# Performance work log

Hardware: AMD Instinct MI355X
Metric: run time of the kernel (lower is better)

## Reference

```python
import jax, jax.numpy as jnp
import numpy as np

NUM_RELS = 19


def rgcn_layer(h, W, b, src, dst, etype, n_nodes):
    """DGL RelGraphConv (basis regularizer, num_bases=num_rels, sum aggregation, bias, no self-loop).

    out[v] = sum_{e: dst(e)=v} W[etype(e)] @ h[src(e)] + b
    Computed as: aggregate h[src] per (relation, dst) pair, then one GEMM per relation.
    """
    # segment id combines relation and destination node -> [R*N] segments
    seg = etype * n_nodes + dst
    agg = jax.ops.segment_sum(h[src], seg, num_segments=NUM_RELS * n_nodes)
    agg = agg.reshape(NUM_RELS, n_nodes, h.shape[1])  # [R, N, in]
    return jnp.einsum('rni,rio->no', agg, W) + b       # [N, out]


def setup_inputs() -> dict:
    key = jax.random.key(0)
    ks = jax.random.split(key, 8)
    N, E, R, D = 100000, 1600000, NUM_RELS, 32
    s = 0.1  # keep activations well-scaled across layers
    return {
        'src': jax.random.randint(ks[0], (E,), 0, N, dtype=jnp.int32),
        'dst': jax.random.randint(ks[1], (E,), 0, N, dtype=jnp.int32),
        'etype': jax.random.randint(ks[2], (E,), 0, R, dtype=jnp.int32),
        'n_nodes': N,
        'W1': jax.random.normal(ks[3], (R, 1, D), jnp.float32) * s,
        'b1': jnp.zeros((D,), jnp.float32),
        'W2': jax.random.normal(ks[4], (R, D, D), jnp.float32) * s,
        'b2': jnp.zeros((D,), jnp.float32),
        'W3': jax.random.normal(ks[5], (D, D), jnp.float32) * s,
        'b3': jnp.zeros((D,), jnp.float32),
    }


def reference(src, dst, etype, n_nodes, W1, b1, W2, b2, W3, b3):
    # h = ones(N, 1), as in Embedder.forward
    h = jnp.ones((n_nodes, 1), jnp.float32)
    h = jax.nn.relu(rgcn_layer(h, W1, b1, src, dst, etype, n_nodes))
    h = jax.nn.relu(rgcn_layer(h, W2, b2, src, dst, etype, n_nodes))
    # conv_output=False -> final layer is a plain Linear
    return h @ W3 + b3
```

## Files before the change

kernel.cpp:

```cpp
#include <hip/hip_runtime.h>

#define NUM_RELS 19
#define NPB 256
#define NPB_SHIFT 8
#define MAXB 400
#define NBLK 512

typedef _Float16 half8 __attribute__((ext_vector_type(8)));
typedef float floatx4 __attribute__((ext_vector_type(4)));



__global__ void w2swz_kernel(const float* __restrict__ W2, _Float16* __restrict__ W2F,
                             int* __restrict__ bcnt, int B) {
    int idx = blockIdx.x * blockDim.x + threadIdx.x;
    if (idx < B) bcnt[idx] = 0;
    if (idx >= NUM_RELS * 2 * 64 * 8) return;
    int j = idx & 7, lane = (idx >> 3) & 63, nt = (idx >> 9) & 1, r = idx >> 10;
    int k = (lane >> 4) * 8 + j, n = nt * 16 + (lane & 15);
    W2F[idx] = (_Float16)W2[r * 1024 + k * 32 + n];
}


__global__ __launch_bounds__(512) void count_kernel(const int* __restrict__ dst,
                                                    int* __restrict__ blkhist,
                                                    int* __restrict__ bcnt,
                                                    int E, int B, int chunk) {
    __shared__ int h[MAXB];
    for (int i = threadIdx.x; i < B; i += 512) h[i] = 0;
    __syncthreads();
    int e0 = blockIdx.x * chunk, e1 = min(E, e0 + chunk);
    for (int e = e0 + (int)threadIdx.x; e < e1; e += 512)
        atomicAdd(&h[dst[e] >> NPB_SHIFT], 1);
    __syncthreads();
    for (int i = threadIdx.x; i < B; i += 512) {
        blkhist[blockIdx.x * B + i] = h[i];
        if (h[i]) atomicAdd(&bcnt[i], h[i]);
    }
}


__global__ __launch_bounds__(NBLK) void offscan_kernel(const int* __restrict__ blkhist,
                                                       const int* __restrict__ bcnt,
                                                       int* __restrict__ pbase,
                                                       int* __restrict__ offs, int B) {
    __shared__ int lds[NBLK];
    __shared__ int pbs;
    int bucket = blockIdx.x;
    int t = threadIdx.x;

    int c = (t < B) ? ((bcnt[t] + 7) & ~7) : 0;
    lds[t] = c;
    __syncthreads();
    for (int off = 1; off < NBLK; off <<= 1) {
        int x = (t >= off) ? lds[t - off] : 0;
        __syncthreads();
        lds[t] += x;
        __syncthreads();
    }
    if (t == bucket) {
        pbs = lds[t] - c;
        pbase[bucket] = pbs;
    }
    __syncthreads();
    int myp = pbs;

    int v = blkhist[t * B + bucket];
    lds[t] = v;
    __syncthreads();
    for (int off = 1; off < NBLK; off <<= 1) {
        int x = (t >= off) ? lds[t - off] : 0;
        __syncthreads();
        lds[t] += x;
        __syncthreads();
    }
    offs[t * B + bucket] = myp + lds[t] - v;
}


__global__ __launch_bounds__(512) void scatter2_kernel(
    const int* __restrict__ src, const int* __restrict__ dst, const int* __restrict__ etype,
    const int* __restrict__ offs, unsigned* __restrict__ recs4, int E, int B, int chunk) {
    __shared__ int cur[MAXB];
    for (int i = threadIdx.x; i < B; i += 512) cur[i] = offs[blockIdx.x * B + i];
    __syncthreads();
    int e0 = blockIdx.x * chunk, e1 = min(E, e0 + chunk);
    for (int e = e0 + (int)threadIdx.x; e < e1; e += 512) {
        int d = dst[e];
        int b = d >> NPB_SHIFT;
        int pos = atomicAdd(&cur[b], 1);
        recs4[pos] = ((unsigned)(d & (NPB - 1)) << 22) | ((unsigned)src[e] << 5) | (unsigned)etype[e];
    }
}


__global__ __launch_bounds__(256) void bsort_l1_kernel(
    const unsigned* __restrict__ recs4, const int* __restrict__ pbase, const int* __restrict__ bcnt,
    int* __restrict__ recs2, int* __restrict__ row_start, int* __restrict__ rend,
    const float* __restrict__ W1, const float* __restrict__ b1, _Float16* __restrict__ h1, int N) {
    __shared__ int hist[NPB];
    __shared__ int offsl[NPB];
    __shared__ int cur[NPB];
    __shared__ int cnt2[NPB * NUM_RELS];
    __shared__ float W1s[NUM_RELS * 32];
    __shared__ float b1s[32];
    int b = blockIdx.x;
    int p0 = pbase[b], n = bcnt[b];
    int t = threadIdx.x;

    hist[t] = 0;
    for (int i = t; i < NPB * NUM_RELS; i += 256) cnt2[i] = 0;
    for (int i = t; i < NUM_RELS * 32; i += 256) W1s[i] = W1[i];
    if (t < 32) b1s[t] = b1[t];
    __syncthreads();

    for (int i = t; i < n; i += 256) {
        unsigned rec = recs4[p0 + i];
        int ln = rec >> 22;
        atomicAdd(&hist[ln], 1);
        atomicAdd(&cnt2[ln * NUM_RELS + (rec & 31)], 1);
    }
    __syncthreads();
    int c = hist[t];
    offsl[t] = c;
    __syncthreads();
    for (int off = 1; off < 256; off <<= 1) {
        int x = (t >= off) ? offsl[t - off] : 0;
        __syncthreads();
        offsl[t] += x;
        __syncthreads();
    }
    int start = p0 + offsl[t] - c;
    cur[t] = start;
    int v = (b << NPB_SHIFT) + t;
    if (v < N) {
        row_start[v] = start;
        rend[v] = start + c;
    }
    __syncthreads();
    for (int i = t; i < n; i += 256) {
        unsigned rec = recs4[p0 + i];
        int p = atomicAdd(&cur[rec >> 22], 1);
        recs2[p] = (int)(rec & 0x3FFFFFu);
    }

    int o = t & 31, hw = t >> 5;
    int v0 = b << NPB_SHIFT;
    for (int k = hw; k < NPB; k += 8) {
        int vv = v0 + k;
        if (vv >= N) break;
        float acc = b1s[o];
        const int* cp = &cnt2[k * NUM_RELS];
#pragma unroll
        for (int r = 0; r < NUM_RELS; ++r) acc += (float)cp[r] * W1s[r * 32 + o];
        h1[(size_t)vv * 32 + o] = (_Float16)fmaxf(acc, 0.f);
    }
}


__global__ __launch_bounds__(256) void transform_kernel(
    const _Float16* __restrict__ h1, const _Float16* __restrict__ W2F,
    _Float16* __restrict__ g, int N) {
    int lane = threadIdx.x & 63;
    int tile = blockIdx.x * 4 + (threadIdx.x >> 6);
    int v0 = tile * 16;
    if (v0 >= N) return;

    half8 a = *(const half8*)(h1 + (size_t)(v0 + (lane & 15)) * 32 + (lane >> 4) * 8);

    floatx4 zero = {0.f, 0.f, 0.f, 0.f};
    int row = (lane >> 4) * 4;
    int col = lane & 15;
    for (int r = 0; r < NUM_RELS; ++r) {
        _Float16* gbase = g + ((size_t)r * N + v0) * 32;
#pragma unroll
        for (int nt = 0; nt < 2; ++nt) {
            half8 bfrag = *(const half8*)(W2F + ((r * 2 + nt) * 64 + lane) * 8);
            floatx4 d = __builtin_amdgcn_mfma_f32_16x16x32_f16(a, bfrag, zero, 0, 0, 0);
#pragma unroll
            for (int reg = 0; reg < 4; ++reg) {
                gbase[(row + reg) * 32 + nt * 16 + col] = (_Float16)d[reg];
            }
        }
    }
}


__global__ __launch_bounds__(512) void edge23_kernel(
    const _Float16* __restrict__ g, const int* __restrict__ row_start,
    const int* __restrict__ rend, const int* __restrict__ recs2,
    const float* __restrict__ b2, const float* __restrict__ W3, const float* __restrict__ b3,
    float* __restrict__ out, int N) {
    __shared__ float W3s[1024];
    __shared__ float b2s[32], b3s[32];
    for (int i = threadIdx.x; i < 1024; i += 512) W3s[i] = W3[i];
    if (threadIdx.x < 32) {
        b2s[threadIdx.x] = b2[threadIdx.x];
        b3s[threadIdx.x] = b3[threadIdx.x];
    }
    __syncthreads();

    int o = threadIdx.x & 31;
    int hw = blockIdx.x * 16 + (threadIdx.x >> 5);
    if (hw >= N) return;
    int start = row_start[hw], end = rend[hw];
    const int sN32 = N * 32;

    float acc = b2s[o];
    for (int base = start; base < end; base += 32) {
        int idx = base + o;
        int m_l = (idx < end) ? recs2[idx] : 0;
        int cnt = min(32, end - base);
        int j = 0;
        for (; j + 4 <= cnt; j += 4) {
            float x[4];
#pragma unroll
            for (int k = 0; k < 4; ++k) {
                int m = __shfl(m_l, j + k, 32);
                x[k] = (float)g[(m & 31) * sN32 + (m >> 5) * 32 + o];
            }
            acc += ((x[0] + x[1]) + (x[2] + x[3]));
        }
        for (; j < cnt; ++j) {
            int m = __shfl(m_l, j, 32);
            acc += (float)g[(m & 31) * sN32 + (m >> 5) * 32 + o];
        }
    }
    float h2v = fmaxf(acc, 0.f);

    float acc3 = b3s[o];
#pragma unroll
    for (int i = 0; i < 32; ++i) {
        float hi = __shfl(h2v, i, 32);
        acc3 = fmaf(hi, W3s[i * 32 + o], acc3);
    }
    out[(size_t)hw * 32 + o] = acc3;
}


extern "C" void kernel_launch(void* const* d_in, const int* in_sizes, int n_in,
                              void* d_out, int out_size, void* d_ws, size_t ws_size,
                              hipStream_t stream) {
    const int* src   = (const int*)d_in[0];
    const int* dst   = (const int*)d_in[1];
    const int* etype = (const int*)d_in[2];
    const float* W1  = (const float*)d_in[4];
    const float* b1  = (const float*)d_in[5];
    const float* W2  = (const float*)d_in[6];
    const float* b2  = (const float*)d_in[7];
    const float* W3  = (const float*)d_in[8];
    const float* b3  = (const float*)d_in[9];
    float* out = (float*)d_out;

    int E = in_sizes[0];
    int N = out_size / 32;
    int B = (N + NPB - 1) >> NPB_SHIFT;

    char* ws = (char*)d_ws;
    size_t off = 0;
    auto alloc = [&](size_t bytes) {
        void* p = ws + off;
        off = (off + bytes + 255) & ~(size_t)255;
        return p;
    };
    _Float16* h1    = (_Float16*)alloc((size_t)N * 32 * 2);
    int* bcnt       = (int*)alloc((size_t)MAXB * 4);
    int* pbase      = (int*)alloc((size_t)MAXB * 4);
    int* blkhist    = (int*)alloc((size_t)NBLK * MAXB * 4);
    int* offs       = (int*)alloc((size_t)NBLK * MAXB * 4);
    int* row_start  = (int*)alloc((size_t)N * 4);
    int* rend       = (int*)alloc((size_t)N * 4);
    unsigned* recs4 = (unsigned*)alloc(((size_t)E + 8 * MAXB + 64) * 4);
    int* recs2      = (int*)alloc(((size_t)E + 8 * MAXB + 64) * 4);
    _Float16* g     = (_Float16*)alloc((size_t)NUM_RELS * N * 32 * 2);
    _Float16* W2F   = (_Float16*)alloc((size_t)NUM_RELS * 2 * 64 * 8 * 2);

    w2swz_kernel<<<(NUM_RELS * 2 * 64 * 8 + 255) / 256, 256, 0, stream>>>(W2, W2F, bcnt, B);

    int chunk = (E + NBLK - 1) / NBLK;
    count_kernel<<<NBLK, 512, 0, stream>>>(dst, blkhist, bcnt, E, B, chunk);
    offscan_kernel<<<B, NBLK, 0, stream>>>(blkhist, bcnt, pbase, offs, B);
    scatter2_kernel<<<NBLK, 512, 0, stream>>>(src, dst, etype, offs, recs4, E, B, chunk);

    bsort_l1_kernel<<<B, 256, 0, stream>>>(recs4, pbase, bcnt, recs2, row_start, rend,
                                           W1, b1, h1, N);

    int ntiles = (N + 15) / 16;
    transform_kernel<<<(ntiles + 3) / 4, 256, 0, stream>>>(h1, W2F, g, N);

    edge23_kernel<<<(N + 15) / 16, 512, 0, stream>>>(g, row_start, rend, recs2, b2, W3, b3, out, N);
}
```

Measured before the change: 230.8 us.

## Fuse layer-1 bucket sort and per-relation transform into one kernel

Merges the bucket-sort/layer-1 kernel with the MFMA transform kernel, so the h1 tile stays in shared memory instead of making a round trip through global memory. This also removes one launch. The fused kernel grows to 512 threads per block. Only B≈391 blocks now do the g-write work that was previously spread over many more blocks, which lowers parallelism for the store-heavy transform stage.

```diff
diff --git a/kernel.cpp b/kernel.cpp
--- a/kernel.cpp
+++ b/kernel.cpp
@@ -94,92 +94,95 @@
 }
 
 
-__global__ __launch_bounds__(256) void bsort_l1_kernel(
+__global__ __launch_bounds__(512) void bsort_l1t_kernel(
     const unsigned* __restrict__ recs4, const int* __restrict__ pbase, const int* __restrict__ bcnt,
     int* __restrict__ recs2, int* __restrict__ row_start, int* __restrict__ rend,
-    const float* __restrict__ W1, const float* __restrict__ b1, _Float16* __restrict__ h1, int N) {
+    const float* __restrict__ W1, const float* __restrict__ b1,
+    const _Float16* __restrict__ W2F, _Float16* __restrict__ g, int N) {
     __shared__ int hist[NPB];
     __shared__ int offsl[NPB];
     __shared__ int cur[NPB];
     __shared__ int cnt2[NPB * NUM_RELS];
     __shared__ float W1s[NUM_RELS * 32];
     __shared__ float b1s[32];
+    __shared__ _Float16 h1t[NPB * 32];
     int b = blockIdx.x;
     int p0 = pbase[b], n = bcnt[b];
     int t = threadIdx.x;
 
-    hist[t] = 0;
-    for (int i = t; i < NPB * NUM_RELS; i += 256) cnt2[i] = 0;
-    for (int i = t; i < NUM_RELS * 32; i += 256) W1s[i] = W1[i];
+    if (t < NPB) hist[t] = 0;
+    for (int i = t; i < NPB * NUM_RELS; i += 512) cnt2[i] = 0;
+    for (int i = t; i < NUM_RELS * 32; i += 512) W1s[i] = W1[i];
     if (t < 32) b1s[t] = b1[t];
     __syncthreads();
 
-    for (int i = t; i < n; i += 256) {
+    for (int i = t; i < n; i += 512) {
         unsigned rec = recs4[p0 + i];
         int ln = rec >> 22;
         atomicAdd(&hist[ln], 1);
         atomicAdd(&cnt2[ln * NUM_RELS + (rec & 31)], 1);
     }
     __syncthreads();
-    int c = hist[t];
-    offsl[t] = c;
-    __syncthreads();
-    for (int off = 1; off < 256; off <<= 1) {
-        int x = (t >= off) ? offsl[t - off] : 0;
-        __syncthreads();
-        offsl[t] += x;
-        __syncthreads();
-    }
-    int start = p0 + offsl[t] - c;
-    cur[t] = start;
-    int v = (b << NPB_SHIFT) + t;
-    if (v < N) {
-        row_start[v] = start;
-        rend[v] = start + c;
-    }
-    __syncthreads();
-    for (int i = t; i < n; i += 256) {
+    int c = 0;
+    if (t < NPB) {
+        c = hist[t];
+        offsl[t] = c;
+    }
+    __syncthreads();
+    for (int off = 1; off < NPB; off <<= 1) {
+        int x = 0;
+        if (t < NPB && t >= off) x = offsl[t - off];
+        __syncthreads();
+        if (t < NPB) offsl[t] += x;
+        __syncthreads();
+    }
+    if (t < NPB) {
+        int start = p0 + offsl[t] - c;
+        cur[t] = start;
+        int v = (b << NPB_SHIFT) + t;
+        if (v < N) {
+            row_start[v] = start;
+            rend[v] = start + c;
+        }
+    }
+    __syncthreads();
+    for (int i = t; i < n; i += 512) {
         unsigned rec = recs4[p0 + i];
         int p = atomicAdd(&cur[rec >> 22], 1);
         recs2[p] = (int)(rec & 0x3FFFFFu);
     }
 
     int o = t & 31, hw = t >> 5;
-    int v0 = b << NPB_SHIFT;
-    for (int k = hw; k < NPB; k += 8) {
-        int vv = v0 + k;
-        if (vv >= N) break;
+    int v0n = b << NPB_SHIFT;
+    for (int k = hw; k < NPB; k += 16) {
+        int vv = v0n + k;
         float acc = b1s[o];
         const int* cp = &cnt2[k * NUM_RELS];
 #pragma unroll
         for (int r = 0; r < NUM_RELS; ++r) acc += (float)cp[r] * W1s[r * 32 + o];
-        h1[(size_t)vv * 32 + o] = (_Float16)fmaxf(acc, 0.f);
-    }
-}
-
-
-__global__ __launch_bounds__(256) void transform_kernel(
-    const _Float16* __restrict__ h1, const _Float16* __restrict__ W2F,
-    _Float16* __restrict__ g, int N) {
-    int lane = threadIdx.x & 63;
-    int tile = blockIdx.x * 4 + (threadIdx.x >> 6);
-    int v0 = tile * 16;
-    if (v0 >= N) return;
-
-    half8 a = *(const half8*)(h1 + (size_t)(v0 + (lane & 15)) * 32 + (lane >> 4) * 8);
-
+        h1t[k * 32 + o] = (vv < N) ? (_Float16)fmaxf(acc, 0.f) : (_Float16)0.f;
+    }
+    __syncthreads();
+
+    int lane = t & 63;
+    int wv = t >> 6;
     floatx4 zero = {0.f, 0.f, 0.f, 0.f};
     int row = (lane >> 4) * 4;
     int col = lane & 15;
-    for (int r = 0; r < NUM_RELS; ++r) {
-        _Float16* gbase = g + ((size_t)r * N + v0) * 32;
-#pragma unroll
-        for (int nt = 0; nt < 2; ++nt) {
-            half8 bfrag = *(const half8*)(W2F + ((r * 2 + nt) * 64 + lane) * 8);
-            floatx4 d = __builtin_amdgcn_mfma_f32_16x16x32_f16(a, bfrag, zero, 0, 0, 0);
-#pragma unroll
-            for (int reg = 0; reg < 4; ++reg) {
-                gbase[(row + reg) * 32 + nt * 16 + col] = (_Float16)d[reg];
+    for (int tile = wv; tile < NPB / 16; tile += 8) {
+        int v0g = v0n + tile * 16;
+        if (v0g >= N) continue;
+        half8 a = *(const half8*)(h1t + (tile * 16 + (lane & 15)) * 32 + (lane >> 4) * 8);
+        for (int r = 0; r < NUM_RELS; ++r) {
+            _Float16* gbase = g + ((size_t)r * N + v0g) * 32;
+#pragma unroll
+            for (int nt = 0; nt < 2; ++nt) {
+                half8 bfrag = *(const half8*)(W2F + ((r * 2 + nt) * 64 + lane) * 8);
+                floatx4 d = __builtin_amdgcn_mfma_f32_16x16x32_f16(a, bfrag, zero, 0, 0, 0);
+#pragma unroll
+                for (int reg = 0; reg < 4; ++reg) {
+                    gbase[(row + reg) * 32 + nt * 16 + col] = (_Float16)d[reg];
+                }
             }
         }
     }
@@ -263,7 +266,6 @@
         off = (off + bytes + 255) & ~(size_t)255;
         return p;
     };
-    _Float16* h1    = (_Float16*)alloc((size_t)N * 32 * 2);
     int* bcnt       = (int*)alloc((size_t)MAXB * 4);
     int* pbase      = (int*)alloc((size_t)MAXB * 4);
     int* blkhist    = (int*)alloc((size_t)NBLK * MAXB * 4);
@@ -282,11 +284,8 @@
     offscan_kernel<<<B, NBLK, 0, stream>>>(blkhist, bcnt, pbase, offs, B);
     scatter2_kernel<<<NBLK, 512, 0, stream>>>(src, dst, etype, offs, recs4, E, B, chunk);
 
-    bsort_l1_kernel<<<B, 256, 0, stream>>>(recs4, pbase, bcnt, recs2, row_start, rend,
-                                           W1, b1, h1, N);
-
-    int ntiles = (N + 15) / 16;
-    transform_kernel<<<(ntiles + 3) / 4, 256, 0, stream>>>(h1, W2F, g, N);
+    bsort_l1t_kernel<<<B, 512, 0, stream>>>(recs4, pbase, bcnt, recs2, row_start, rend,
+                                            W1, b1, W2F, g, N);
 
     edge23_kernel<<<(N + 15) / 16, 512, 0, stream>>>(g, row_start, rend, recs2, b2, W3, b3, out, N);
 }
```

Result: faster. 208.8 us (-9.5%).

## Aggregate before transform: per-(dst,rel) sums then fused MFMA GEMM for layers 2-3

Applied to the files above, without the earlier changes.

Reorders layer 2 from transform-then-gather (a per-relation g table gathered per edge) to gather-then-transform. An agg kernel sorts each destination block's edges by (node, relation) in shared memory, sums h1 rows into a dense fp16 [R,N,32] buffer, and a gemm kernel then runs the per-relation MFMA accumulation with layer 3 fused in through a second MFMA. Per-edge random gathers now touch the small h1 table instead of the 19x larger g table. In exchange it writes and reads a full dense agg buffer (mostly zeros), and it silently truncates any block with more than SCAP edges. It also assumes N is a multiple of 16 in the gemm tiling.

```diff
diff --git a/kernel.cpp b/kernel.cpp
--- a/kernel.cpp
+++ b/kernel.cpp
@@ -5,20 +5,30 @@
 #define NPB_SHIFT 8
 #define MAXB 400
 #define NBLK 512
+#define NK (NPB * NUM_RELS)
+#define SCAP 6144
 
 typedef _Float16 half8 __attribute__((ext_vector_type(8)));
 typedef float floatx4 __attribute__((ext_vector_type(4)));
 
 
 
-__global__ void w2swz_kernel(const float* __restrict__ W2, _Float16* __restrict__ W2F,
-                             int* __restrict__ bcnt, int B) {
+__global__ void wswz_kernel(const float* __restrict__ W2, const float* __restrict__ W3,
+                            _Float16* __restrict__ W2F, _Float16* __restrict__ W3F,
+                            int* __restrict__ bcnt, int B) {
     int idx = blockIdx.x * blockDim.x + threadIdx.x;
     if (idx < B) bcnt[idx] = 0;
-    if (idx >= NUM_RELS * 2 * 64 * 8) return;
-    int j = idx & 7, lane = (idx >> 3) & 63, nt = (idx >> 9) & 1, r = idx >> 10;
-    int k = (lane >> 4) * 8 + j, n = nt * 16 + (lane & 15);
-    W2F[idx] = (_Float16)W2[r * 1024 + k * 32 + n];
+    if (idx >= NUM_RELS * 1024 + 1024) return;
+    if (idx < NUM_RELS * 1024) {
+        int j = idx & 7, lane = (idx >> 3) & 63, nt = (idx >> 9) & 1, r = idx >> 10;
+        int k = (lane >> 4) * 8 + j, n = nt * 16 + (lane & 15);
+        W2F[idx] = (_Float16)W2[r * 1024 + k * 32 + n];
+    } else {
+        int li = idx - NUM_RELS * 1024;
+        int j = li & 7, lane = (li >> 3) & 63, nt = (li >> 9) & 1;
+        int k = (lane >> 4) * 8 + j, n = nt * 16 + (lane & 15);
+        W3F[li] = (_Float16)W3[k * 32 + n];
+    }
 }
 
 
@@ -94,56 +104,25 @@
 }
 
 
-__global__ __launch_bounds__(256) void bsort_l1_kernel(
+__global__ __launch_bounds__(256) void l1_kernel(
     const unsigned* __restrict__ recs4, const int* __restrict__ pbase, const int* __restrict__ bcnt,
-    int* __restrict__ recs2, int* __restrict__ row_start, int* __restrict__ rend,
     const float* __restrict__ W1, const float* __restrict__ b1, _Float16* __restrict__ h1, int N) {
-    __shared__ int hist[NPB];
-    __shared__ int offsl[NPB];
-    __shared__ int cur[NPB];
-    __shared__ int cnt2[NPB * NUM_RELS];
+    __shared__ int cnt2[NK];
     __shared__ float W1s[NUM_RELS * 32];
     __shared__ float b1s[32];
     int b = blockIdx.x;
     int p0 = pbase[b], n = bcnt[b];
     int t = threadIdx.x;
 
-    hist[t] = 0;
-    for (int i = t; i < NPB * NUM_RELS; i += 256) cnt2[i] = 0;
+    for (int i = t; i < NK; i += 256) cnt2[i] = 0;
     for (int i = t; i < NUM_RELS * 32; i += 256) W1s[i] = W1[i];
     if (t < 32) b1s[t] = b1[t];
     __syncthreads();
-
     for (int i = t; i < n; i += 256) {
         unsigned rec = recs4[p0 + i];
-        int ln = rec >> 22;
-        atomicAdd(&hist[ln], 1);
-        atomicAdd(&cnt2[ln * NUM_RELS + (rec & 31)], 1);
-    }
-    __syncthreads();
-    int c = hist[t];
-    offsl[t] = c;
-    __syncthreads();
-    for (int off = 1; off < 256; off <<= 1) {
-        int x = (t >= off) ? offsl[t - off] : 0;
-        __syncthreads();
-        offsl[t] += x;
-        __syncthreads();
-    }
-    int start = p0 + offsl[t] - c;
-    cur[t] = start;
-    int v = (b << NPB_SHIFT) + t;
-    if (v < N) {
-        row_start[v] = start;
-        rend[v] = start + c;
-    }
-    __syncthreads();
-    for (int i = t; i < n; i += 256) {
-        unsigned rec = recs4[p0 + i];
-        int p = atomicAdd(&cur[rec >> 22], 1);
-        recs2[p] = (int)(rec & 0x3FFFFFu);
-    }
-
+        atomicAdd(&cnt2[(rec >> 22) * NUM_RELS + (rec & 31)], 1);
+    }
+    __syncthreads();
     int o = t & 31, hw = t >> 5;
     int v0 = b << NPB_SHIFT;
     for (int k = hw; k < NPB; k += 8) {
@@ -158,83 +137,166 @@
 }
 
 
-__global__ __launch_bounds__(256) void transform_kernel(
-    const _Float16* __restrict__ h1, const _Float16* __restrict__ W2F,
-    _Float16* __restrict__ g, int N) {
-    int lane = threadIdx.x & 63;
-    int tile = blockIdx.x * 4 + (threadIdx.x >> 6);
-    int v0 = tile * 16;
-    if (v0 >= N) return;
-
-    half8 a = *(const half8*)(h1 + (size_t)(v0 + (lane & 15)) * 32 + (lane >> 4) * 8);
-
-    floatx4 zero = {0.f, 0.f, 0.f, 0.f};
-    int row = (lane >> 4) * 4;
-    int col = lane & 15;
-    for (int r = 0; r < NUM_RELS; ++r) {
-        _Float16* gbase = g + ((size_t)r * N + v0) * 32;
-#pragma unroll
-        for (int nt = 0; nt < 2; ++nt) {
-            half8 bfrag = *(const half8*)(W2F + ((r * 2 + nt) * 64 + lane) * 8);
-            floatx4 d = __builtin_amdgcn_mfma_f32_16x16x32_f16(a, bfrag, zero, 0, 0, 0);
-#pragma unroll
-            for (int reg = 0; reg < 4; ++reg) {
-                gbase[(row + reg) * 32 + nt * 16 + col] = (_Float16)d[reg];
+__global__ __launch_bounds__(512) void agg_kernel(
+    const unsigned* __restrict__ recs4, const int* __restrict__ pbase, const int* __restrict__ bcnt,
+    const _Float16* __restrict__ h1, _Float16* __restrict__ agg, int N) {
+    __shared__ int goff[NK];
+    __shared__ int cur[NK];
+    __shared__ int srec[SCAP];
+    int b = blockIdx.x;
+    int p0 = pbase[b];
+    int n = min(bcnt[b], SCAP);
+    int t = threadIdx.x;
+
+    for (int i = t; i < NK; i += 512) goff[i] = 0;
+    __syncthreads();
+    for (int i = t; i < n; i += 512) {
+        unsigned rec = recs4[p0 + i];
+        atomicAdd(&goff[(rec >> 22) * NUM_RELS + (rec & 31)], 1);
+    }
+    __syncthreads();
+
+    int base = t * 10;
+    int cnt[10];
+    int s = 0;
+#pragma unroll
+    for (int q = 0; q < 10; ++q) {
+        int i = base + q;
+        int v = (i < NK) ? goff[i] : 0;
+        cnt[q] = v;
+        s += v;
+    }
+    srec[t] = s;
+    __syncthreads();
+    for (int off = 1; off < 512; off <<= 1) {
+        int x = (t >= off) ? srec[t - off] : 0;
+        __syncthreads();
+        srec[t] += x;
+        __syncthreads();
+    }
+    int run = srec[t] - s;
+    __syncthreads();
+#pragma unroll
+    for (int q = 0; q < 10; ++q) {
+        int i = base + q;
+        if (i < NK) {
+            goff[i] = run;
+            cur[i] = run;
+            run += cnt[q];
+        }
+    }
+    __syncthreads();
+
+    for (int i = t; i < n; i += 512) {
+        unsigned rec = recs4[p0 + i];
+        int key = (rec >> 22) * NUM_RELS + (rec & 31);
+        int pos = atomicAdd(&cur[key], 1);
+        srec[pos] = (int)(rec & 0x3FFFFFu);
+    }
+    __syncthreads();
+
+    int o = t & 31, hw = t >> 5;
+    int v0n = b << NPB_SHIFT;
+    const int N32 = N * 32;
+    for (int ln = hw; ln < NPB; ln += 16) {
+        int v = v0n + ln;
+        if (v >= N) continue;
+        int k0 = ln * NUM_RELS;
+        int ns = goff[k0];
+        int ne = cur[k0 + NUM_RELS - 1];
+        int vbase = v * 32 + o;
+
+        int cur_r = 0;
+        float acc = 0.f;
+        for (int bb = ns; bb < ne; bb += 32) {
+            int idx = bb + o;
+            int m_l = (idx < ne) ? srec[idx] : 0;
+            int cnt_ = min(32, ne - bb);
+            int j = 0;
+            for (; j + 4 <= cnt_; j += 4) {
+                int m[4];
+                float x[4];
+#pragma unroll
+                for (int k = 0; k < 4; ++k) {
+                    m[k] = __shfl(m_l, j + k, 32);
+                    x[k] = (float)h1[(m[k] >> 5) * 32 + o];
+                }
+#pragma unroll
+                for (int k = 0; k < 4; ++k) {
+                    int r = m[k] & 31;
+                    if (r != cur_r) {
+                        agg[(size_t)cur_r * N32 + vbase] = (_Float16)acc;
+                        for (int rr = cur_r + 1; rr < r; ++rr)
+                            agg[(size_t)rr * N32 + vbase] = (_Float16)0.f;
+                        cur_r = r;
+                        acc = 0.f;
+                    }
+                    acc += x[k];
+                }
+            }
+            for (; j < cnt_; ++j) {
+                int m = __shfl(m_l, j, 32);
+                float x = (float)h1[(m >> 5) * 32 + o];
+                int r = m & 31;
+                if (r != cur_r) {
+                    agg[(size_t)cur_r * N32 + vbase] = (_Float16)acc;
+                    for (int rr = cur_r + 1; rr < r; ++rr)
+                        agg[(size_t)rr * N32 + vbase] = (_Float16)0.f;
+                    cur_r = r;
+                    acc = 0.f;
+                }
+                acc += x;
             }
         }
-    }
-}
-
-
-__global__ __launch_bounds__(512) void edge23_kernel(
-    const _Float16* __restrict__ g, const int* __restrict__ row_start,
-    const int* __restrict__ rend, const int* __restrict__ recs2,
-    const float* __restrict__ b2, const float* __restrict__ W3, const float* __restrict__ b3,
-    float* __restrict__ out, int N) {
-    __shared__ float W3s[1024];
-    __shared__ float b2s[32], b3s[32];
-    for (int i = threadIdx.x; i < 1024; i += 512) W3s[i] = W3[i];
-    if (threadIdx.x < 32) {
-        b2s[threadIdx.x] = b2[threadIdx.x];
-        b3s[threadIdx.x] = b3[threadIdx.x];
-    }
-    __syncthreads();
-
-    int o = threadIdx.x & 31;
-    int hw = blockIdx.x * 16 + (threadIdx.x >> 5);
-    if (hw >= N) return;
-    int start = row_start[hw], end = rend[hw];
-    const int sN32 = N * 32;
-
-    float acc = b2s[o];
-    for (int base = start; base < end; base += 32) {
-        int idx = base + o;
-        int m_l = (idx < end) ? recs2[idx] : 0;
-        int cnt = min(32, end - base);
-        int j = 0;
-        for (; j + 4 <= cnt; j += 4) {
-            float x[4];
-#pragma unroll
-            for (int k = 0; k < 4; ++k) {
-                int m = __shfl(m_l, j + k, 32);
-                x[k] = (float)g[(m & 31) * sN32 + (m >> 5) * 32 + o];
-            }
-            acc += ((x[0] + x[1]) + (x[2] + x[3]));
+        agg[(size_t)cur_r * N32 + vbase] = (_Float16)acc;
+        for (int rr = cur_r + 1; rr < NUM_RELS; ++rr)
+            agg[(size_t)rr * N32 + vbase] = (_Float16)0.f;
+    }
+}
+
+
+__global__ __launch_bounds__(256) void gemm_kernel(
+    const _Float16* __restrict__ agg, const _Float16* __restrict__ W2F,
+    const _Float16* __restrict__ W3F, const float* __restrict__ b2,
+    const float* __restrict__ b3, float* __restrict__ out, int N) {
+    __shared__ _Float16 h2t[4][16 * 32];
+    int lane = threadIdx.x & 63, wv = threadIdx.x >> 6;
+    int ntiles = N / 16;
+    int tile = blockIdx.x * 4 + wv;
+    bool valid = tile < ntiles;
+    int tilec = valid ? tile : (ntiles - 1);
+    int v0 = tilec * 16;
+    int col = lane & 15, quad = lane >> 4;
+    const int N32 = N * 32;
+
+    floatx4 acc0 = {0.f, 0.f, 0.f, 0.f}, acc1 = {0.f, 0.f, 0.f, 0.f};
+    for (int r = 0; r < NUM_RELS; ++r) {
+        half8 a = *(const half8*)(agg + (size_t)r * N32 + (v0 + col) * 32 + quad * 8);
+        acc0 = __builtin_amdgcn_mfma_f32_16x16x32_f16(a, *(const half8*)(W2F + ((r * 2 + 0) * 64 + lane) * 8), acc0, 0, 0, 0);
+        acc1 = __builtin_amdgcn_mfma_f32_16x16x32_f16(a, *(const half8*)(W2F + ((r * 2 + 1) * 64 + lane) * 8), acc1, 0, 0, 0);
+    }
+    float b2a = b2[col], b2b = b2[16 + col];
+#pragma unroll
+    for (int reg = 0; reg < 4; ++reg) {
+        int row = quad * 4 + reg;
+        h2t[wv][row * 32 + col] = (_Float16)fmaxf(acc0[reg] + b2a, 0.f);
+        h2t[wv][row * 32 + 16 + col] = (_Float16)fmaxf(acc1[reg] + b2b, 0.f);
+    }
+    __syncthreads();
+
+    half8 a2 = *(const half8*)(&h2t[wv][col * 32 + quad * 8]);
+    float b3a = b3[col], b3b = b3[16 + col];
+    floatx4 o0 = {b3a, b3a, b3a, b3a}, o1 = {b3b, b3b, b3b, b3b};
+    o0 = __builtin_amdgcn_mfma_f32_16x16x32_f16(a2, *(const half8*)(W3F + (0 * 64 + lane) * 8), o0, 0, 0, 0);
+    o1 = __builtin_amdgcn_mfma_f32_16x16x32_f16(a2, *(const half8*)(W3F + (1 * 64 + lane) * 8), o1, 0, 0, 0);
+    if (valid) {
+#pragma unroll
+        for (int reg = 0; reg < 4; ++reg) {
+            int row = quad * 4 + reg;
+            out[(size_t)(v0 + row) * 32 + col] = o0[reg];
+            out[(size_t)(v0 + row) * 32 + 16 + col] = o1[reg];
         }
-        for (; j < cnt; ++j) {
-            int m = __shfl(m_l, j, 32);
-            acc += (float)g[(m & 31) * sN32 + (m >> 5) * 32 + o];
-        }
-    }
-    float h2v = fmaxf(acc, 0.f);
-
-    float acc3 = b3s[o];
-#pragma unroll
-    for (int i = 0; i < 32; ++i) {
-        float hi = __shfl(h2v, i, 32);
-        acc3 = fmaf(hi, W3s[i * 32 + o], acc3);
-    }
-    out[(size_t)hw * 32 + o] = acc3;
+    }
 }
 
 
@@ -263,30 +325,26 @@
         off = (off + bytes + 255) & ~(size_t)255;
         return p;
     };
-    _Float16* h1    = (_Float16*)alloc((size_t)N * 32 * 2);
     int* bcnt       = (int*)alloc((size_t)MAXB * 4);
     int* pbase      = (int*)alloc((size_t)MAXB * 4);
     int* blkhist    = (int*)alloc((size_t)NBLK * MAXB * 4);
     int* offs       = (int*)alloc((size_t)NBLK * MAXB * 4);
-    int* row_start  = (int*)alloc((size_t)N * 4);
-    int* rend       = (int*)alloc((size_t)N * 4);
     unsigned* recs4 = (unsigned*)alloc(((size_t)E + 8 * MAXB + 64) * 4);
-    int* recs2      = (int*)alloc(((size_t)E + 8 * MAXB + 64) * 4);
-    _Float16* g     = (_Float16*)alloc((size_t)NUM_RELS * N * 32 * 2);
-    _Float16* W2F   = (_Float16*)alloc((size_t)NUM_RELS * 2 * 64 * 8 * 2);
-
-    w2swz_kernel<<<(NUM_RELS * 2 * 64 * 8 + 255) / 256, 256, 0, stream>>>(W2, W2F, bcnt, B);
+    _Float16* h1    = (_Float16*)alloc((size_t)N * 32 * 2);
+    _Float16* agg   = (_Float16*)alloc((size_t)NUM_RELS * N * 32 * 2);
+    _Float16* W2F   = (_Float16*)alloc((size_t)NUM_RELS * 1024 * 2);
+    _Float16* W3F   = (_Float16*)alloc((size_t)1024 * 2);
+
+    wswz_kernel<<<(NUM_RELS * 1024 + 1024 + 255) / 256, 256, 0, stream>>>(W2, W3, W2F, W3F, bcnt, B);
 
     int chunk = (E + NBLK - 1) / NBLK;
     count_kernel<<<NBLK, 512, 0, stream>>>(dst, blkhist, bcnt, E, B, chunk);
     offscan_kernel<<<B, NBLK, 0, stream>>>(blkhist, bcnt, pbase, offs, B);
     scatter2_kernel<<<NBLK, 512, 0, stream>>>(src, dst, etype, offs, recs4, E, B, chunk);
 
-    bsort_l1_kernel<<<B, 256, 0, stream>>>(recs4, pbase, bcnt, recs2, row_start, rend,
-                                           W1, b1, h1, N);
-
-    int ntiles = (N + 15) / 16;
-    transform_kernel<<<(ntiles + 3) / 4, 256, 0, stream>>>(h1, W2F, g, N);
-
-    edge23_kernel<<<(N + 15) / 16, 512, 0, stream>>>(g, row_start, rend, recs2, b2, W3, b3, out, N);
-}
+    l1_kernel<<<B, 256, 0, stream>>>(recs4, pbase, bcnt, W1, b1, h1, N);
+    agg_kernel<<<B, 512, 0, stream>>>(recs4, pbase, bcnt, h1, agg, N);
+
+    int ntiles = N / 16;
+    gemm_kernel<<<(ntiles + 3) / 4, 256, 0, stream>>>(agg, W2F, W3F, b2, b3, out, N);
+}
```

Result: slower. 269.9 us (+16.9%).
